# Optimization experiments

Measured on AMD Instinct MI355X. Metric: run time of the kernel, lower is better.

## Reference

```python
import jax, jax.numpy as jnp
import numpy as np

D = 128   # hidden_dims
H = 8     # head_num
ALPHA = 0.5
EPS = 1e-5


def setup_inputs() -> dict:
    key = jax.random.key(0)
    ks = jax.random.split(key, 16)
    B, S = 2, 2048
    s = 0.02
    inp = {
        'x': jax.random.normal(ks[0], (B, S, D), jnp.float32),
        'adj_matrix': jax.random.randint(ks[1], (S, S), 0, 2, jnp.int32),
        'Wq': jax.random.normal(ks[2], (D, D * H), jnp.float32) * s,
        'bq': jnp.zeros((D * H,), jnp.float32),
        'Wk': jax.random.normal(ks[3], (D, D * H), jnp.float32) * s,
        'bk': jnp.zeros((D * H,), jnp.float32),
        'Wv': jax.random.normal(ks[4], (D, D * H), jnp.float32) * s,
        'bv': jnp.zeros((D * H,), jnp.float32),
        'Wo': jax.random.normal(ks[5], (D * H, D), jnp.float32) * s,
        'bo': jnp.zeros((D,), jnp.float32),
        'g1': jnp.ones((D,), jnp.float32), 'be1': jnp.zeros((D,), jnp.float32),
        'g2': jnp.ones((D,), jnp.float32), 'be2': jnp.zeros((D,), jnp.float32),
        'W1': jax.random.normal(ks[6], (D, D), jnp.float32) * s,
        'b1': jnp.zeros((D,), jnp.float32),
        'W2': jax.random.normal(ks[7], (D, D), jnp.float32) * s,
        'b2': jnp.zeros((D,), jnp.float32),
    }
    return inp


def _layernorm(x, g, b):
    mu = jnp.mean(x, axis=-1, keepdims=True)
    var = jnp.var(x, axis=-1, keepdims=True)
    return (x - mu) * jax.lax.rsqrt(var + EPS) * g + b


def reference(x, adj_matrix, Wq, bq, Wk, bk, Wv, bv, Wo, bo, g1, be1, g2, be2, W1, b1, W2, b2):
    B, S, _ = x.shape
    q = (x @ Wq + bq).reshape(B, S, H, D)
    k = (x @ Wk + bk).reshape(B, S, H, D)
    v = (x @ Wv + bv).reshape(B, S, H, D)
    scores = jnp.einsum('bqhd,bkhd->bhqk', q, k) / jnp.sqrt(jnp.float32(D))
    soft_mask = ALPHA * adj_matrix.astype(jnp.float32) + (1.0 - ALPHA)  # [S,S]
    scores = scores * soft_mask  # broadcast over B,H
    attn = jax.nn.softmax(scores, axis=-1)
    out = jnp.einsum('bhqk,bkhd->bqhd', attn, v).reshape(B, S, H * D)
    out = out @ Wo + bo
    h = _layernorm(x + out, g1, be1)
    ff = jax.nn.relu(h @ W1 + b1) @ W2 + b2
    y = _layernorm(h + ff, g2, be2)
    return y, attn
```

## Files before the change

kernel.cpp:

```cpp
#include <hip/hip_runtime.h>
#include <hip/hip_bf16.h>

#define HD 128
#define NH 8
#define SQ 2048
#define NROWS 4096
#define RSQRT_D 0.08838834764831845f
#define L2EH 0.72134752044f

typedef __bf16 bf16;
typedef bf16 bf16x8 __attribute__((ext_vector_type(8)));
typedef float f32x4 __attribute__((ext_vector_type(4)));

__device__ __forceinline__ f32x4 mfma16(bf16x8 a, bf16x8 b, f32x4 c) {
  return __builtin_amdgcn_mfma_f32_16x16x32_bf16(a, b, c, 0, 0, 0);
}
__device__ __forceinline__ bf16x8 ld8(const bf16* p) { return *(const bf16x8*)p; }
__device__ __forceinline__ unsigned short bfu(float v) {
  return __builtin_bit_cast(unsigned short, (bf16)v);
}
__device__ __forceinline__ unsigned packbf2(float a, float b) {
  return (unsigned)bfu(a) | ((unsigned)bfu(b) << 16);
}
__device__ __forceinline__ void gload_lds16(const void* g, void* l) {
  __builtin_amdgcn_global_load_lds(
      (const __attribute__((address_space(1))) void*)g,
      (__attribute__((address_space(3))) void*)l, 16, 0, 0);
}

__global__ void k_prep_a(const float* __restrict__ x, const int* __restrict__ adj,
                         bf16* __restrict__ xb, unsigned char* __restrict__ mask8) {
  int idx = blockIdx.x * 256 + threadIdx.x;
  if (idx < NROWS * HD) { xb[idx] = (bf16)x[idx]; return; }
  int j = idx - NROWS * HD;
  if (j < (SQ * SQ / 4)) {
    int4 a = ((const int4*)adj)[j];
    uchar4 m;
    m.x = (unsigned char)a.x; m.y = (unsigned char)a.y;
    m.z = (unsigned char)a.z; m.w = (unsigned char)a.w;
    ((uchar4*)mask8)[j] = m;
  }
}

__global__ void k_prep_w(const float* __restrict__ Wq, const float* __restrict__ Wk,
                         const float* __restrict__ Wv, const float* __restrict__ Wo,
                         const float* __restrict__ W1, const float* __restrict__ W2,
                         bf16* __restrict__ WqkvT, bf16* __restrict__ WoT,
                         bf16* __restrict__ W1T, bf16* __restrict__ W2T) {
  int idx = blockIdx.x * 256 + threadIdx.x;
  if (idx < 3072 * 128) {
    int n = idx >> 7, kk = idx & 127;
    int sel = n >> 10, nn = n & 1023;
    const float* W = (sel == 0) ? Wq : (sel == 1 ? Wk : Wv);
    WqkvT[idx] = (bf16)W[kk * 1024 + nn];
    return;
  }
  int j = idx - 3072 * 128;
  if (j < 128 * 1024) { int n = j >> 10, kk = j & 1023; WoT[j] = (bf16)Wo[kk * 128 + n]; return; }
  j -= 128 * 1024;
  if (j < 16384) { int n = j >> 7, kk = j & 127; W1T[j] = (bf16)W1[kk * 128 + n]; return; }
  j -= 16384;
  if (j < 16384) { int n = j >> 7, kk = j & 127; W2T[j] = (bf16)W2[kk * 128 + n]; return; }
}

__global__ __launch_bounds__(256, 4) void k_qkv(
    const bf16* __restrict__ xb, const bf16* __restrict__ WqkvT,
    const float* __restrict__ bq, const float* __restrict__ bk, const float* __restrict__ bv,
    bf16* __restrict__ qT, bf16* __restrict__ kT, bf16* __restrict__ vT) {
  const int bid = blockIdx.x;
  const int m0 = (bid & 63) << 6;
  const int n0 = (bid >> 6) << 6;
  const int tid = threadIdx.x;
  const int w = tid >> 6, lane = tid & 63, lo = lane & 15, hi = lane >> 4;
  const int mw = m0 + ((w >> 1) << 5);
  const int nw = n0 + ((w & 1) << 5);
  bf16x8 av[2][4], bw[2][4];
#pragma unroll
  for (int ms = 0; ms < 2; ++ms)
#pragma unroll
    for (int ks = 0; ks < 4; ++ks)
      av[ms][ks] = ld8(xb + (size_t)(mw + ms * 16 + lo) * 128 + ks * 32 + hi * 8);
#pragma unroll
  for (int ns = 0; ns < 2; ++ns)
#pragma unroll
    for (int ks = 0; ks < 4; ++ks)
      bw[ns][ks] = ld8(WqkvT + (size_t)(nw + ns * 16 + lo) * 128 + ks * 32 + hi * 8);
  const f32x4 z4 = {0.f, 0.f, 0.f, 0.f};
  f32x4 acc[2][2] = {{z4, z4}, {z4, z4}};
#pragma unroll
  for (int ms = 0; ms < 2; ++ms)
#pragma unroll
    for (int ns = 0; ns < 2; ++ns)
#pragma unroll
      for (int ks = 0; ks < 4; ++ks)
        acc[ms][ns] = mfma16(av[ms][ks], bw[ns][ks], acc[ms][ns]);
#pragma unroll
  for (int ns = 0; ns < 2; ++ns) {
    const int n = nw + ns * 16 + lo;
    const int sel = n >> 10, nn = n & 1023;
    const float bia = (sel == 0 ? bq : sel == 1 ? bk : bv)[nn];
    const int hh = nn >> 7, d = nn & 127;
#pragma unroll
    for (int ms = 0; ms < 2; ++ms) {
      const int mb = mw + ms * 16 + hi * 4;
      const int bb = mb >> 11, s = mb & 2047;
      if (sel == 0) {
#pragma unroll
        for (int r = 0; r < 4; ++r)
          qT[(size_t)((bb * 8 + hh) * 2048 + s + r) * 128 + d] =
              (bf16)((acc[ms][ns][r] + bia) * RSQRT_D);
      } else if (sel == 1) {
#pragma unroll
        for (int r = 0; r < 4; ++r)
          kT[(size_t)((bb * 8 + hh) * 2048 + s + r) * 128 + d] = (bf16)(acc[ms][ns][r] + bia);
      } else {
        ushort4 pk;
        pk.x = bfu(acc[ms][ns][0] + bia);
        pk.y = bfu(acc[ms][ns][1] + bia);
        pk.z = bfu(acc[ms][ns][2] + bia);
        pk.w = bfu(acc[ms][ns][3] + bia);
        *(ushort4*)(vT + (size_t)((bb * 8 + hh) * 128 + d) * 2048 + s) = pk;
      }
    }
  }
}

__global__ __launch_bounds__(256, 2) void k_attn(
    const bf16* __restrict__ qT, const bf16* __restrict__ kT,
    const bf16* __restrict__ vT, const unsigned char* __restrict__ mask8,
    float* __restrict__ attn_out, bf16* __restrict__ Oc) {
  __shared__ __align__(16) char kbuf[2][8192];
  __shared__ __align__(16) char vbuf[2][8192];
  __shared__ __align__(16) char stash[4][1024];
  __shared__ float red2[64];

  const int lbid = blockIdx.x;
  const int work = ((lbid & 7) << 6) + (lbid >> 3);
  const int bh = work >> 5;
  const int q0 = (work & 31) << 6;
  const int b = bh >> 3, h = bh & 7;
  const int tid = threadIdx.x;
  const int w = tid >> 6, lane = tid & 63, lo = lane & 15, hi = lane >> 4;

  const bf16* Qh = qT + (size_t)bh * SQ * HD;
  const bf16* Kh = kT + (size_t)bh * SQ * HD;
  const bf16* Vh = vT + (size_t)bh * HD * SQ;
  const int qg = q0 + w * 16 + lo;

  const int krow0 = (w << 2) + (lane >> 4);
  const int krow1 = 16 + krow0;
  const bf16* kg0 = Kh + (size_t)krow0 * HD + (((lane & 15) ^ (krow0 & 7)) << 3);
  const bf16* kg1 = Kh + (size_t)krow1 * HD + (((lane & 15) ^ (krow1 & 7)) << 3);
  const int vrow0 = (w << 4) + (lane >> 2);
  const int vrow1 = 64 + vrow0;
  const bf16* vg0 = Vh + (size_t)vrow0 * SQ + ((lane & 3) << 3);
  const bf16* vg1 = Vh + (size_t)vrow1 * SQ + ((lane & 3) << 3);

  bf16x8 qf[4];
#pragma unroll
  for (int ks = 0; ks < 4; ++ks)
    qf[ks] = ld8(Qh + (size_t)qg * HD + ks * 32 + hi * 8);

  const f32x4 z4 = {0.f, 0.f, 0.f, 0.f};
  f32x4 acc[8];
#pragma unroll
  for (int ds = 0; ds < 8; ++ds) acc[ds] = z4;
  float ssum = 0.f;

  gload_lds16(kg0, &kbuf[0][w * 1024]);
  gload_lds16(kg1, &kbuf[0][4096 + w * 1024]);
  gload_lds16(vg0, &vbuf[0][w * 1024]);
  gload_lds16(vg1, &vbuf[0][4096 + w * 1024]);
  __syncthreads();

  for (int i = 0; i < 64; ++i) {
    const int kvA = i << 5;
    const int cur = i & 1;
    if (i < 63) {
      const size_t ko = (size_t)(kvA + 32) * HD;
      gload_lds16(kg0 + ko, &kbuf[cur ^ 1][w * 1024]);
      gload_lds16(kg1 + ko, &kbuf[cur ^ 1][4096 + w * 1024]);
      gload_lds16(vg0 + (kvA + 32), &vbuf[cur ^ 1][w * 1024]);
      gload_lds16(vg1 + (kvA + 32), &vbuf[cur ^ 1][4096 + w * 1024]);
    }
    const char* kb = kbuf[cur];
    const char* vb = vbuf[cur];
#pragma unroll
    for (int t = 0; t < 2; ++t) {
      const int row = t * 16 + lo;
      bf16x8 af[4];
#pragma unroll
      for (int ks = 0; ks < 4; ++ks)
        af[ks] = *(const bf16x8*)(kb + row * 256 + ((((ks << 2) + hi)) ^ (row & 7)) * 16);
      f32x4 c = z4;
#pragma unroll
      for (int ks = 0; ks < 4; ++ks) c = mfma16(af[ks], qf[ks], c);
      const unsigned mu = *(const unsigned*)(mask8 + (size_t)qg * SQ + kvA + t * 16 + hi * 4);
      float p0 = exp2f(c[0] * fmaf((float)(mu & 0xff),         L2EH, L2EH));
      float p1 = exp2f(c[1] * fmaf((float)((mu >> 8) & 0xff),  L2EH, L2EH));
      float p2 = exp2f(c[2] * fmaf((float)((mu >> 16) & 0xff), L2EH, L2EH));
      float p3 = exp2f(c[3] * fmaf((float)((mu >> 24) & 0xff), L2EH, L2EH));
      ssum += (p0 + p1) + (p2 + p3);
      *(uint2*)(stash[w] + lo * 64 + ((t * 32 + hi * 8) ^ ((lo & 3) << 4))) =
          make_uint2(packbf2(p0, p1), packbf2(p2, p3));
    }
    bf16x8 pa = *(const bf16x8*)(stash[w] + lo * 64 + ((hi * 16) ^ ((lo & 3) << 4)));
#pragma unroll
    for (int ds = 0; ds < 8; ++ds) {
      bf16x8 vf = *(const bf16x8*)(vb + (ds * 16 + lo) * 64 + hi * 16);
      acc[ds] = mfma16(pa, vf, acc[ds]);
    }
    __syncthreads();
  }

  ssum += __shfl_xor(ssum, 16);
  ssum += __shfl_xor(ssum, 32);
  if (hi == 0) red2[w * 16 + lo] = 1.0f / ssum;
  __syncthreads();

#pragma unroll
  for (int ds = 0; ds < 8; ++ds)
#pragma unroll
    for (int r = 0; r < 4; ++r) {
      const int qrow = w * 16 + hi * 4 + r;
      Oc[(size_t)(b * SQ + q0 + qrow) * (NH * HD) + h * HD + ds * 16 + lo] =
          (bf16)(acc[ds][r] * red2[qrow]);
    }

  const float rinv = red2[w * 16 + lo];
  float* abase = attn_out + (size_t)bh * SQ * SQ + (size_t)qg * SQ;
  gload_lds16(kg0, &kbuf[0][w * 1024]);
  gload_lds16(kg1, &kbuf[0][4096 + w * 1024]);
  __syncthreads();
  for (int i = 0; i < 64; ++i) {
    const int kvA = i << 5;
    const int cur = i & 1;
    if (i < 63) {
      const size_t ko = (size_t)(kvA + 32) * HD;
      gload_lds16(kg0 + ko, &kbuf[cur ^ 1][w * 1024]);
      gload_lds16(kg1 + ko, &kbuf[cur ^ 1][4096 + w * 1024]);
    }
    const char* kb = kbuf[cur];
#pragma unroll
    for (int t = 0; t < 2; ++t) {
      const int row = t * 16 + lo;
      bf16x8 af[4];
#pragma unroll
      for (int ks = 0; ks < 4; ++ks)
        af[ks] = *(const bf16x8*)(kb + row * 256 + ((((ks << 2) + hi)) ^ (row & 7)) * 16);
      f32x4 c = z4;
#pragma unroll
      for (int ks = 0; ks < 4; ++ks) c = mfma16(af[ks], qf[ks], c);
      const unsigned mu = *(const unsigned*)(mask8 + (size_t)qg * SQ + kvA + t * 16 + hi * 4);
      f32x4 o;
      o[0] = exp2f(c[0] * fmaf((float)(mu & 0xff),         L2EH, L2EH)) * rinv;
      o[1] = exp2f(c[1] * fmaf((float)((mu >> 8) & 0xff),  L2EH, L2EH)) * rinv;
      o[2] = exp2f(c[2] * fmaf((float)((mu >> 16) & 0xff), L2EH, L2EH)) * rinv;
      o[3] = exp2f(c[3] * fmaf((float)((mu >> 24) & 0xff), L2EH, L2EH)) * rinv;
      __builtin_nontemporal_store(o, (f32x4*)(abase + kvA + t * 16 + hi * 4));
    }
    __syncthreads();
  }
}

__global__ __launch_bounds__(256, 4) void k_owo(
    const bf16* __restrict__ Oc, const bf16* __restrict__ WoT,
    const float* __restrict__ bo, const float* __restrict__ x,
    const float* __restrict__ g1, const float* __restrict__ be1,
    float* __restrict__ hf, bf16* __restrict__ hb) {
  __shared__ __align__(16) float hbuf[16 * 128];
  const int m0 = blockIdx.x * 16;
  const int tid = threadIdx.x;
  const int w = tid >> 6, lane = tid & 63, lo = lane & 15, hi = lane >> 4;
  const int nw = w * 32;
  const f32x4 z4 = {0.f, 0.f, 0.f, 0.f};
  f32x4 acc[2] = {z4, z4};
#pragma unroll 4
  for (int kk = 0; kk < 32; ++kk) {
    bf16x8 a = ld8(Oc + (size_t)(m0 + lo) * 1024 + kk * 32 + hi * 8);
#pragma unroll
    for (int ns = 0; ns < 2; ++ns) {
      bf16x8 bb = ld8(WoT + (size_t)(nw + ns * 16 + lo) * 1024 + kk * 32 + hi * 8);
      acc[ns] = mfma16(a, bb, acc[ns]);
    }
  }
#pragma unroll
  for (int ns = 0; ns < 2; ++ns) {
    const int n = nw + ns * 16 + lo;
    const float bia = bo[n];
#pragma unroll
    for (int r = 0; r < 4; ++r) {
      const int mr = hi * 4 + r;
      hbuf[mr * 128 + n] = acc[ns][r] + bia + x[(size_t)(m0 + mr) * 128 + n];
    }
  }
  __syncthreads();
  const float2 g = *(const float2*)(g1 + lane * 2);
  const float2 be = *(const float2*)(be1 + lane * 2);
#pragma unroll
  for (int rr = 0; rr < 4; ++rr) {
    const int row = w * 4 + rr;
    float2 v = *(float2*)&hbuf[row * 128 + lane * 2];
    float s = v.x + v.y, sq = v.x * v.x + v.y * v.y;
#pragma unroll
    for (int off = 32; off; off >>= 1) { s += __shfl_xor(s, off); sq += __shfl_xor(sq, off); }
    const float mean = s * (1.f / 128.f);
    const float var = sq * (1.f / 128.f) - mean * mean;
    const float rstd = rsqrtf(var + 1e-5f);
    const float y0 = (v.x - mean) * rstd * g.x + be.x;
    const float y1 = (v.y - mean) * rstd * g.y + be.y;
    const size_t o = (size_t)(m0 + row) * 128 + lane * 2;
    *(float2*)(hf + o) = make_float2(y0, y1);
    *(unsigned*)(hb + o) = packbf2(y0, y1);
  }
}

__global__ __launch_bounds__(256, 4) void k_ffn(
    const bf16* __restrict__ hb, const float* __restrict__ hf,
    const bf16* __restrict__ W1T, const bf16* __restrict__ W2T,
    const float* __restrict__ b1, const float* __restrict__ b2,
    const float* __restrict__ g2, const float* __restrict__ be2,
    float* __restrict__ yout) {
  __shared__ __align__(16) bf16 s1[16 * 136];
  __shared__ __align__(16) float ybuf[16 * 128];
  const int m0 = blockIdx.x * 16;
  const int tid = threadIdx.x;
  const int w = tid >> 6, lane = tid & 63, lo = lane & 15, hi = lane >> 4;
  const int nw = w * 32;
  const f32x4 z4 = {0.f, 0.f, 0.f, 0.f};
  f32x4 a1[2] = {z4, z4};
#pragma unroll
  for (int kk = 0; kk < 4; ++kk) {
    bf16x8 a = ld8(hb + (size_t)(m0 + lo) * 128 + kk * 32 + hi * 8);
#pragma unroll
    for (int ns = 0; ns < 2; ++ns)
      a1[ns] = mfma16(a, ld8(W1T + (size_t)(nw + ns * 16 + lo) * 128 + kk * 32 + hi * 8), a1[ns]);
  }
#pragma unroll
  for (int ns = 0; ns < 2; ++ns) {
    const int n = nw + ns * 16 + lo;
    const float bia = b1[n];
#pragma unroll
    for (int r = 0; r < 4; ++r)
      s1[(hi * 4 + r) * 136 + n] = (bf16)fmaxf(a1[ns][r] + bia, 0.f);
  }
  __syncthreads();
  f32x4 a2[2] = {z4, z4};
#pragma unroll
  for (int kk = 0; kk < 4; ++kk) {
    bf16x8 a = *(const bf16x8*)&s1[lo * 136 + kk * 32 + hi * 8];
#pragma unroll
    for (int ns = 0; ns < 2; ++ns)
      a2[ns] = mfma16(a, ld8(W2T + (size_t)(nw + ns * 16 + lo) * 128 + kk * 32 + hi * 8), a2[ns]);
  }
#pragma unroll
  for (int ns = 0; ns < 2; ++ns) {
    const int n = nw + ns * 16 + lo;
    const float bia = b2[n];
#pragma unroll
    for (int r = 0; r < 4; ++r) {
      const int mr = hi * 4 + r;
      ybuf[mr * 128 + n] = a2[ns][r] + bia + hf[(size_t)(m0 + mr) * 128 + n];
    }
  }
  __syncthreads();
  const float2 g = *(const float2*)(g2 + lane * 2);
  const float2 be = *(const float2*)(be2 + lane * 2);
#pragma unroll
  for (int rr = 0; rr < 4; ++rr) {
    const int row = w * 4 + rr;
    float2 v = *(float2*)&ybuf[row * 128 + lane * 2];
    float s = v.x + v.y, sq = v.x * v.x + v.y * v.y;
#pragma unroll
    for (int off = 32; off; off >>= 1) { s += __shfl_xor(s, off); sq += __shfl_xor(sq, off); }
    const float mean = s * (1.f / 128.f);
    const float var = sq * (1.f / 128.f) - mean * mean;
    const float rstd = rsqrtf(var + 1e-5f);
    const float y0 = (v.x - mean) * rstd * g.x + be.x;
    const float y1 = (v.y - mean) * rstd * g.y + be.y;
    *(float2*)(yout + (size_t)(m0 + row) * 128 + lane * 2) = make_float2(y0, y1);
  }
}

extern "C" void kernel_launch(void* const* d_in, const int* in_sizes, int n_in,
                              void* d_out, int out_size, void* d_ws, size_t ws_size,
                              hipStream_t stream) {
  const float* x  = (const float*)d_in[0];
  const int* adj  = (const int*)d_in[1];
  const float* Wq = (const float*)d_in[2];  const float* bq = (const float*)d_in[3];
  const float* Wk = (const float*)d_in[4];  const float* bk = (const float*)d_in[5];
  const float* Wv = (const float*)d_in[6];  const float* bv = (const float*)d_in[7];
  const float* Wo = (const float*)d_in[8];  const float* bo = (const float*)d_in[9];
  const float* g1 = (const float*)d_in[10]; const float* be1 = (const float*)d_in[11];
  const float* g2 = (const float*)d_in[12]; const float* be2 = (const float*)d_in[13];
  const float* W1 = (const float*)d_in[14]; const float* b1 = (const float*)d_in[15];
  const float* W2 = (const float*)d_in[16]; const float* b2 = (const float*)d_in[17];

  char* ws = (char*)d_ws;
  bf16* xb     = (bf16*)(ws + 0);
  bf16* WqkvT  = (bf16*)(ws + 1048576);
  bf16* WoT    = (bf16*)(ws + 1835008);
  bf16* W1T    = (bf16*)(ws + 2097152);
  bf16* W2T    = (bf16*)(ws + 2129920);
  unsigned char* mask8 = (unsigned char*)(ws + 2162688);
  bf16* qT     = (bf16*)(ws + 6356992);
  bf16* kT     = (bf16*)(ws + 14745600);
  bf16* vT     = (bf16*)(ws + 23134208);
  bf16* Oc     = (bf16*)(ws + 31522816);
  float* hf    = (float*)(ws + 39911424);
  bf16* hb     = (bf16*)(ws + 42008576);

  float* yout = (float*)d_out;
  float* attn_out = yout + (size_t)NROWS * HD;

  k_prep_a<<<6144, 256, 0, stream>>>(x, adj, xb, mask8);
  k_prep_w<<<2176, 256, 0, stream>>>(Wq, Wk, Wv, Wo, W1, W2, WqkvT, WoT, W1T, W2T);
  k_qkv<<<3072, 256, 0, stream>>>(xb, WqkvT, bq, bk, bv, qT, kT, vT);
  k_attn<<<512, 256, 0, stream>>>(qT, kT, vT, mask8, attn_out, Oc);
  k_owo<<<256, 256, 0, stream>>>(Oc, WoT, bo, x, g1, be1, hf, hb);
  k_ffn<<<256, 256, 0, stream>>>(hb, hf, W1T, W2T, b1, b2, g2, be2, yout);
}
```

Baseline: 209.8 us.

## Bit-pack adjacency mask, stage it via LDS, fold softmax scaling into Q

The adjacency mask is packed into one bit per key instead of one byte, which shrinks the preprocessing write and the per-tile mask reads in both attention passes. Each tile's 32-bit mask words are now loaded asynchronously into LDS alongside K and V. The 0.5·log2(e)/sqrt(D) factor moves into the Q projection, so the exponent becomes a single fma. The final normalisation is folded into the exp2 argument as log2(1/sum) instead of a separate multiply. s_setprio is also raised around the PV MFMA block. The changes add bit-extract ALU work per element and assume adjacency values are 0/1.

Measured after the change: 218.9 us. +4.3%, slower.

```diff
diff --git a/kernel.cpp b/kernel.cpp
--- a/kernel.cpp
+++ b/kernel.cpp
@@ -6,7 +6,7 @@
 #define SQ 2048
 #define NROWS 4096
 #define RSQRT_D 0.08838834764831845f
-#define L2EH 0.72134752044f
+#define QSCALE 0.06375871607f
 
 typedef __bf16 bf16;
 typedef bf16 bf16x8 __attribute__((ext_vector_type(8)));
@@ -27,18 +27,30 @@
       (const __attribute__((address_space(1))) void*)g,
       (__attribute__((address_space(3))) void*)l, 16, 0, 0);
 }
+__device__ __forceinline__ void gload_lds4(const void* g, void* l) {
+  __builtin_amdgcn_global_load_lds(
+      (const __attribute__((address_space(1))) void*)g,
+      (__attribute__((address_space(3))) void*)l, 4, 0, 0);
+}
 
 __global__ void k_prep_a(const float* __restrict__ x, const int* __restrict__ adj,
-                         bf16* __restrict__ xb, unsigned char* __restrict__ mask8) {
+                         bf16* __restrict__ xb, unsigned* __restrict__ maskb) {
   int idx = blockIdx.x * 256 + threadIdx.x;
   if (idx < NROWS * HD) { xb[idx] = (bf16)x[idx]; return; }
   int j = idx - NROWS * HD;
-  if (j < (SQ * SQ / 4)) {
-    int4 a = ((const int4*)adj)[j];
-    uchar4 m;
-    m.x = (unsigned char)a.x; m.y = (unsigned char)a.y;
-    m.z = (unsigned char)a.z; m.w = (unsigned char)a.w;
-    ((uchar4*)mask8)[j] = m;
+  if (j < SQ * (SQ / 32)) {
+    const int q = j >> 6, wd = j & 63;
+    const int4* base = (const int4*)(adj + (size_t)q * SQ + wd * 32);
+    unsigned bits = 0;
+#pragma unroll
+    for (int kq = 0; kq < 8; ++kq) {
+      int4 a = base[kq];
+      bits |= (unsigned)(a.x != 0) << (kq * 4 + 0);
+      bits |= (unsigned)(a.y != 0) << (kq * 4 + 1);
+      bits |= (unsigned)(a.z != 0) << (kq * 4 + 2);
+      bits |= (unsigned)(a.w != 0) << (kq * 4 + 3);
+    }
+    maskb[j] = bits;
   }
 }
 
@@ -108,7 +120,7 @@
 #pragma unroll
         for (int r = 0; r < 4; ++r)
           qT[(size_t)((bb * 8 + hh) * 2048 + s + r) * 128 + d] =
-              (bf16)((acc[ms][ns][r] + bia) * RSQRT_D);
+              (bf16)((acc[ms][ns][r] + bia) * QSCALE);
       } else if (sel == 1) {
 #pragma unroll
         for (int r = 0; r < 4; ++r)
@@ -127,11 +139,12 @@
 
 __global__ __launch_bounds__(256, 2) void k_attn(
     const bf16* __restrict__ qT, const bf16* __restrict__ kT,
-    const bf16* __restrict__ vT, const unsigned char* __restrict__ mask8,
+    const bf16* __restrict__ vT, const unsigned* __restrict__ maskb,
     float* __restrict__ attn_out, bf16* __restrict__ Oc) {
   __shared__ __align__(16) char kbuf[2][8192];
   __shared__ __align__(16) char vbuf[2][8192];
   __shared__ __align__(16) char stash[4][1024];
+  __shared__ unsigned mbuf[2][64];
   __shared__ float red2[64];
 
   const int lbid = blockIdx.x;
@@ -146,6 +159,7 @@
   const bf16* Kh = kT + (size_t)bh * SQ * HD;
   const bf16* Vh = vT + (size_t)bh * HD * SQ;
   const int qg = q0 + w * 16 + lo;
+  const unsigned* mrow = maskb + (size_t)(q0 + lane) * 64;
 
   const int krow0 = (w << 2) + (lane >> 4);
   const int krow1 = 16 + krow0;
@@ -171,6 +185,7 @@
   gload_lds16(kg1, &kbuf[0][4096 + w * 1024]);
   gload_lds16(vg0, &vbuf[0][w * 1024]);
   gload_lds16(vg1, &vbuf[0][4096 + w * 1024]);
+  if (w == 0) gload_lds4(mrow, &mbuf[0][0]);
   __syncthreads();
 
   for (int i = 0; i < 64; ++i) {
@@ -182,9 +197,11 @@
       gload_lds16(kg1 + ko, &kbuf[cur ^ 1][4096 + w * 1024]);
       gload_lds16(vg0 + (kvA + 32), &vbuf[cur ^ 1][w * 1024]);
       gload_lds16(vg1 + (kvA + 32), &vbuf[cur ^ 1][4096 + w * 1024]);
+      if (w == 0) gload_lds4(mrow + i + 1, &mbuf[cur ^ 1][0]);
     }
     const char* kb = kbuf[cur];
     const char* vb = vbuf[cur];
+    const unsigned mu32 = mbuf[cur][w * 16 + lo];
 #pragma unroll
     for (int t = 0; t < 2; ++t) {
       const int row = t * 16 + lo;
@@ -195,21 +212,22 @@
       f32x4 c = z4;
 #pragma unroll
       for (int ks = 0; ks < 4; ++ks) c = mfma16(af[ks], qf[ks], c);
-      const unsigned mu = *(const unsigned*)(mask8 + (size_t)qg * SQ + kvA + t * 16 + hi * 4);
-      float p0 = exp2f(c[0] * fmaf((float)(mu & 0xff),         L2EH, L2EH));
-      float p1 = exp2f(c[1] * fmaf((float)((mu >> 8) & 0xff),  L2EH, L2EH));
-      float p2 = exp2f(c[2] * fmaf((float)((mu >> 16) & 0xff), L2EH, L2EH));
-      float p3 = exp2f(c[3] * fmaf((float)((mu >> 24) & 0xff), L2EH, L2EH));
+      float p0 = exp2f(fmaf(c[0], (float)((mu32 >> (t * 16 + hi * 4 + 0)) & 1), c[0]));
+      float p1 = exp2f(fmaf(c[1], (float)((mu32 >> (t * 16 + hi * 4 + 1)) & 1), c[1]));
+      float p2 = exp2f(fmaf(c[2], (float)((mu32 >> (t * 16 + hi * 4 + 2)) & 1), c[2]));
+      float p3 = exp2f(fmaf(c[3], (float)((mu32 >> (t * 16 + hi * 4 + 3)) & 1), c[3]));
       ssum += (p0 + p1) + (p2 + p3);
       *(uint2*)(stash[w] + lo * 64 + ((t * 32 + hi * 8) ^ ((lo & 3) << 4))) =
           make_uint2(packbf2(p0, p1), packbf2(p2, p3));
     }
     bf16x8 pa = *(const bf16x8*)(stash[w] + lo * 64 + ((hi * 16) ^ ((lo & 3) << 4)));
+    __builtin_amdgcn_s_setprio(1);
 #pragma unroll
     for (int ds = 0; ds < 8; ++ds) {
       bf16x8 vf = *(const bf16x8*)(vb + (ds * 16 + lo) * 64 + hi * 16);
       acc[ds] = mfma16(pa, vf, acc[ds]);
     }
+    __builtin_amdgcn_s_setprio(0);
     __syncthreads();
   }
 
@@ -228,9 +246,11 @@
     }
 
   const float rinv = red2[w * 16 + lo];
+  const float lr = log2f(rinv);
   float* abase = attn_out + (size_t)bh * SQ * SQ + (size_t)qg * SQ;
   gload_lds16(kg0, &kbuf[0][w * 1024]);
   gload_lds16(kg1, &kbuf[0][4096 + w * 1024]);
+  if (w == 0) gload_lds4(mrow, &mbuf[0][0]);
   __syncthreads();
   for (int i = 0; i < 64; ++i) {
     const int kvA = i << 5;
@@ -239,8 +259,10 @@
       const size_t ko = (size_t)(kvA + 32) * HD;
       gload_lds16(kg0 + ko, &kbuf[cur ^ 1][w * 1024]);
       gload_lds16(kg1 + ko, &kbuf[cur ^ 1][4096 + w * 1024]);
+      if (w == 0) gload_lds4(mrow + i + 1, &mbuf[cur ^ 1][0]);
     }
     const char* kb = kbuf[cur];
+    const unsigned mu32 = mbuf[cur][w * 16 + lo];
 #pragma unroll
     for (int t = 0; t < 2; ++t) {
       const int row = t * 16 + lo;
@@ -251,12 +273,11 @@
       f32x4 c = z4;
 #pragma unroll
       for (int ks = 0; ks < 4; ++ks) c = mfma16(af[ks], qf[ks], c);
-      const unsigned mu = *(const unsigned*)(mask8 + (size_t)qg * SQ + kvA + t * 16 + hi * 4);
       f32x4 o;
-      o[0] = exp2f(c[0] * fmaf((float)(mu & 0xff),         L2EH, L2EH)) * rinv;
-      o[1] = exp2f(c[1] * fmaf((float)((mu >> 8) & 0xff),  L2EH, L2EH)) * rinv;
-      o[2] = exp2f(c[2] * fmaf((float)((mu >> 16) & 0xff), L2EH, L2EH)) * rinv;
-      o[3] = exp2f(c[3] * fmaf((float)((mu >> 24) & 0xff), L2EH, L2EH)) * rinv;
+      o[0] = exp2f(fmaf(c[0], (float)((mu32 >> (t * 16 + hi * 4 + 0)) & 1), c[0] + lr));
+      o[1] = exp2f(fmaf(c[1], (float)((mu32 >> (t * 16 + hi * 4 + 1)) & 1), c[1] + lr));
+      o[2] = exp2f(fmaf(c[2], (float)((mu32 >> (t * 16 + hi * 4 + 2)) & 1), c[2] + lr));
+      o[3] = exp2f(fmaf(c[3], (float)((mu32 >> (t * 16 + hi * 4 + 3)) & 1), c[3] + lr));
       __builtin_nontemporal_store(o, (f32x4*)(abase + kvA + t * 16 + hi * 4));
     }
     __syncthreads();
@@ -402,7 +423,7 @@
   bf16* WoT    = (bf16*)(ws + 1835008);
   bf16* W1T    = (bf16*)(ws + 2097152);
   bf16* W2T    = (bf16*)(ws + 2129920);
-  unsigned char* mask8 = (unsigned char*)(ws + 2162688);
+  unsigned* maskb = (unsigned*)(ws + 2162688);
   bf16* qT     = (bf16*)(ws + 6356992);
   bf16* kT     = (bf16*)(ws + 14745600);
   bf16* vT     = (bf16*)(ws + 23134208);
@@ -413,10 +434,10 @@
   float* yout = (float*)d_out;
   float* attn_out = yout + (size_t)NROWS * HD;
 
-  k_prep_a<<<6144, 256, 0, stream>>>(x, adj, xb, mask8);
+  k_prep_a<<<2560, 256, 0, stream>>>(x, adj, xb, maskb);
   k_prep_w<<<2176, 256, 0, stream>>>(Wq, Wk, Wv, Wo, W1, W2, WqkvT, WoT, W1T, W2T);
   k_qkv<<<3072, 256, 0, stream>>>(xb, WqkvT, bq, bk, bv, qT, kT, vT);
-  k_attn<<<512, 256, 0, stream>>>(qT, kT, vT, mask8, attn_out, Oc);
+  k_attn<<<512, 256, 0, stream>>>(qT, kT, vT, maskb, attn_out, Oc);
   k_owo<<<256, 256, 0, stream>>>(Oc, WoT, bo, x, g1, be1, hf, hb);
   k_ffn<<<256, 256, 0, stream>>>(hb, hf, W1T, W2T, b1, b2, g2, be2, yout);
 }
```
